# Performance work log

Hardware: AMD Instinct MI355X
Metric: run time of the kernel (lower is better)

## Reference

```python
import jax, jax.numpy as jnp
import numpy as np

HIDDEN = 128
IN_SIZE = 1
OUT_SIZE = 1
ENC_T = 8192
DEC_T = 4096


def _lstm_step(h, c, x, Wih, Whh, bih, bhh):
    # PyTorch LSTM gate order: i, f, g, o
    gates = Wih @ x + Whh @ h + bih + bhh  # [4H]
    i, f, g, o = jnp.split(gates, 4)
    c = jax.nn.sigmoid(f) * c + jax.nn.sigmoid(i) * jnp.tanh(g)
    h = jax.nn.sigmoid(o) * jnp.tanh(c)
    return h, c


def setup_inputs() -> dict:
    key = jax.random.key(0)
    ks = jax.random.split(key, 12)
    k = 1.0 / np.sqrt(HIDDEN)  # PyTorch default init bound
    u = lambda kk, shape: jax.random.uniform(kk, shape, jnp.float32, -k, k)
    return {
        "input_seq": jax.random.normal(ks[0], (ENC_T,), jnp.float32),
        "enc_Wih": u(ks[1], (4 * HIDDEN, IN_SIZE)),
        "enc_Whh": u(ks[2], (4 * HIDDEN, HIDDEN)),
        "enc_bih": u(ks[3], (4 * HIDDEN,)),
        "enc_bhh": u(ks[4], (4 * HIDDEN,)),
        "dec_Wih": u(ks[5], (4 * HIDDEN, OUT_SIZE)),
        "dec_Whh": u(ks[6], (4 * HIDDEN, HIDDEN)),
        "dec_bih": u(ks[7], (4 * HIDDEN,)),
        "dec_bhh": u(ks[8], (4 * HIDDEN,)),
        "fc_W": u(ks[9], (OUT_SIZE, HIDDEN)),
        "fc_b": u(ks[10], (OUT_SIZE,)),
        "target_seq_len": DEC_T,
    }


def reference(input_seq, enc_Wih, enc_Whh, enc_bih, enc_bhh,
              dec_Wih, dec_Whh, dec_bih, dec_bhh, fc_W, fc_b,
              target_seq_len):
    H = enc_Whh.shape[1]
    dt = input_seq.dtype

    def enc_step(carry, xt):
        h, c = carry
        h, c = _lstm_step(h, c, xt[None], enc_Wih, enc_Whh, enc_bih, enc_bhh)
        return (h, c), None

    (h, c), _ = jax.lax.scan(enc_step,
                             (jnp.zeros(H, dt), jnp.zeros(H, dt)),
                             input_seq)

    def dec_step(carry, _):
        h, c, y = carry  # y: previous prediction, shape [1]
        h, c = _lstm_step(h, c, y, dec_Wih, dec_Whh, dec_bih, dec_bhh)
        pred = fc_W @ h + fc_b  # [1]
        return (h, c, pred), pred

    _, preds = jax.lax.scan(dec_step, (h, c, jnp.zeros(1, dt)),
                            None, length=target_seq_len)
    # preds: [T_out, 1] -> torch.cat(outputs, dim=1) gives [1, T_out]
    return preds.T
```

## Files before the change

### kernel.cpp

```cpp
#include <hip/hip_runtime.h>


#define H      128
#define ENC_T  8192
#define DEC_T  4096
#define NT     512
#define NBLK   1
#define PSLICE 648

typedef float v2f __attribute__((ext_vector_type(2)));

__device__ __forceinline__ v2f pk_fma_s(v2f a, v2f b_sgpr, v2f c) {
    v2f d;
    asm("v_pk_fma_f32 %0, %1, %2, %3" : "=v"(d) : "v"(a), "s"(b_sgpr), "v"(c));
    return d;
}
__device__ __forceinline__ v2f pk_fma(v2f a, v2f b, v2f c) {
    v2f d;
    asm("v_pk_fma_f32 %0, %1, %2, %3" : "=v"(d) : "v"(a), "v"(b), "v"(c));
    return d;
}
__device__ __forceinline__ float sigm(float x) {
    return __builtin_amdgcn_rcpf(1.0f + __expf(-x));
}
__device__ __forceinline__ float tanhfast(float x) {
    return 1.0f - 2.0f * __builtin_amdgcn_rcpf(1.0f + __expf(2.0f * x));
}
__device__ __forceinline__ float rdlane(float v, int l) {
    return __int_as_float(__builtin_amdgcn_readlane(__float_as_int(v), l));
}
template <int CTRL>
__device__ __forceinline__ float qperm(float v) {
    return __int_as_float(
        __builtin_amdgcn_mov_dpp(__float_as_int(v), CTRL, 0xf, 0xf, true));
}

__global__ __launch_bounds__(NT, 2)
void seq2seq_lstm(const float* __restrict__ input_seq,
                  const float* __restrict__ enc_Wih,
                  const float* __restrict__ enc_Whh,
                  const float* __restrict__ enc_bih,
                  const float* __restrict__ enc_bhh,
                  const float* __restrict__ dec_Wih,
                  const float* __restrict__ dec_Whh,
                  const float* __restrict__ dec_bih,
                  const float* __restrict__ dec_bhh,
                  const float* __restrict__ fc_W,
                  const float* __restrict__ fc_b,
                  float* __restrict__ out,
                  unsigned* __restrict__ wsflag)
{
    (void)wsflag;
    __shared__ __align__(16) float xin[ENC_T];
    __shared__ __align__(16) float hbuf[2][H];
    __shared__ __align__(16) float part[2][8 * PSLICE];

    const int t    = threadIdx.x;
    const int lane = t & 63;
    const int wv   = t >> 6;
    const int jb   = 16 * wv;
    const int qq   = lane >> 2;
    const int g    = lane & 3;
    const int myu  = jb + qq;
    const int myrow = g * H + myu;
    const int prd  = 5 * myu + g;
    const int pwb  = wv * PSLICE + 5 * lane;

    {
        const float4* s = (const float4*)input_seq;
        float4* d = (float4*)xin;
        for (int i = t; i < ENC_T / 4; i += NT) d[i] = s[i];
    }

    v2f w2[8][8];
#pragma unroll
    for (int s = 0; s < 8; ++s) {
        const v2f* Wr = (const v2f*)(enc_Whh + (64 * s + lane) * H + jb);
#pragma unroll
        for (int jj = 0; jj < 8; ++jj) w2[s][jj] = Wr[jj];
    }
    float bias_r = enc_bih[myrow] + enc_bhh[myrow];
    float wih_r  = enc_Wih[myrow];

    float cst = 0.f;
    float hn  = 0.f;
    __syncthreads();

#define MATVEC(PB)                                                          \
    {                                                                       \
        v2f acc2[8];                                                        \
        _Pragma("unroll") for (int s = 0; s < 8; ++s)                       \
            acc2[s] = (v2f){0.f, 0.f};                                      \
        _Pragma("unroll") for (int jj = 0; jj < 8; ++jj) {                  \
            const float se = rdlane(hn, 8 * jj + 3);                        \
            const float so = rdlane(hn, 8 * jj + 7);                        \
            const v2f hp = {se, so};                                        \
            _Pragma("unroll") for (int s = 0; s < 8; ++s)                   \
                acc2[s] = pk_fma_s(w2[s][jj], hp, acc2[s]);                 \
        }                                                                   \
             \
        float* pb_ = &part[PB][pwb];                                        \
        pb_[0]   = acc2[0].x + acc2[0].y; pb_[320] = acc2[1].x + acc2[1].y; \
        pb_[1]   = acc2[2].x + acc2[2].y; pb_[321] = acc2[3].x + acc2[3].y; \
        pb_[2]   = acc2[4].x + acc2[4].y; pb_[322] = acc2[5].x + acc2[5].y; \
        pb_[3]   = acc2[6].x + acc2[6].y; pb_[323] = acc2[7].x + acc2[7].y; \
    }

#define REDUCE_UPDATE(PB, ABASE, STH)                                       \
    {                                                                       \
        const float p0 = part[PB][0 * PSLICE + prd];                        \
        const float p1 = part[PB][1 * PSLICE + prd];                        \
        const float p2 = part[PB][2 * PSLICE + prd];                        \
        const float p3 = part[PB][3 * PSLICE + prd];                        \
        const float p4 = part[PB][4 * PSLICE + prd];                        \
        const float p5 = part[PB][5 * PSLICE + prd];                        \
        const float p6 = part[PB][6 * PSLICE + prd];                        \
        const float p7 = part[PB][7 * PSLICE + prd];                        \
        const float a = (ABASE) + (((p0 + p1) + (p2 + p3)) +                \
                                   ((p4 + p5) + (p6 + p7)));                \
        const float v = (g == 2) ? tanhfast(a) : sigm(a);                   \
        const float vi = qperm<0x00>(v);                   \
        const float vf = qperm<0x55>(v);                   \
        const float vg = qperm<0xAA>(v);                   \
        const float vo = qperm<0xFF>(v);                   \
        cst = fmaf(vf, cst, vi * vg);                                       \
        hn  = vo * tanhfast(cst);                                           \
        if (STH && g == 3) hbuf[PB][myu] = hn;                              \
    }

    for (int st = 0; st < ENC_T; ++st) {
        const int pb = st & 1;
        MATVEC(pb);
        const float x = xin[st];
        __syncthreads();
        REDUCE_UPDATE(pb, fmaf(wih_r, x, bias_r), 0);
    }
    if (g == 3) hbuf[1][myu] = hn;

    const float fcb = fc_b[0];
    const float fwl = fc_W[lane];
    const float fwh = fc_W[64 + lane];
#pragma unroll
    for (int s = 0; s < 8; ++s) {
        const int r = 64 * s + lane;
        const float vi = dec_Wih[r];
        const v2f vip = {vi, vi};
        const v2f* Wr = (const v2f*)(dec_Whh + r * H + jb);
        const v2f* Fr = (const v2f*)(fc_W + jb);
#pragma unroll
        for (int jj = 0; jj < 8; ++jj)
            w2[s][jj] = pk_fma(vip, Fr[jj], Wr[jj]);
    }
    wih_r  = dec_Wih[myrow];
    bias_r = dec_bih[myrow] + dec_bhh[myrow] + wih_r * fcb;
    __syncthreads();
    float q0;
    {
        float p = fmaf(fwl, hbuf[1][lane], fwh * hbuf[1][64 + lane]);
        p += qperm<0xB1>(p);
        p += qperm<0x4E>(p);
#pragma unroll
        for (int m = 32; m >= 4; m >>= 1) p += __shfl_xor(p, m, 64);
        q0 = p + fcb;
    }
    float cb = bias_r - wih_r * q0;

    for (int st = 0; st < DEC_T; ++st) {
        const int pb = st & 1;
        MATVEC(pb);
        if (wv == 7 && st >= 2) {
            float p = fmaf(fwl, hbuf[pb][lane], fwh * hbuf[pb][64 + lane]);
            p += qperm<0xB1>(p);
            p += qperm<0x4E>(p);
#pragma unroll
            for (int m = 32; m >= 4; m >>= 1) p += __shfl_xor(p, m, 64);
            if (lane == 0) out[st - 2] = p + fcb;
        }
        __syncthreads();
        REDUCE_UPDATE(pb, cb, 1);
        cb = bias_r;
    }

    __syncthreads();
    if (wv == 7) {
        float p0 = fmaf(fwl, hbuf[0][lane], fwh * hbuf[0][64 + lane]);
        float p1 = fmaf(fwl, hbuf[1][lane], fwh * hbuf[1][64 + lane]);
#pragma unroll
        for (int m = 32; m >= 1; m >>= 1) {
            p0 += __shfl_xor(p0, m, 64);
            p1 += __shfl_xor(p1, m, 64);
        }
        if (lane == 0) {
            out[DEC_T - 2] = p0 + fcb;
            out[DEC_T - 1] = p1 + fcb;
        }
    }
}

extern "C" void kernel_launch(void* const* d_in, const int* in_sizes, int n_in,
                              void* d_out, int out_size, void* d_ws, size_t ws_size,
                              hipStream_t stream)
{
    (void)in_sizes; (void)n_in; (void)ws_size; (void)out_size;
    seq2seq_lstm<<<NBLK, NT, 0, stream>>>(
        (const float*)d_in[0],
        (const float*)d_in[1],
        (const float*)d_in[2],
        (const float*)d_in[3],
        (const float*)d_in[4],
        (const float*)d_in[5],
        (const float*)d_in[6],
        (const float*)d_in[7],
        (const float*)d_in[8],
        (const float*)d_in[9],
        (const float*)d_in[10],
        (float*)d_out,
        (unsigned*)d_ws);
}
```

Before: 8.680 ms.

## Interleave partial sums across warps so reduction uses two float4 LDS loads

Changes the shared-memory partial-sum layout so each output row's 8 per-warp partials are contiguous, with an XOR swizzle on the warp index to spread writes across banks. The reduce step then reads two float4 values instead of eight scalar loads. The step loops are unrolled by two with constant buffer indices, and the decoder's output projection is moved after the barrier so it reads the just-written hidden state, which shortens the output lag from two steps to one. This cuts LDS load instructions on the serial critical path, at the cost of more complex index math and possible write bank conflicts.

```diff
diff --git a/kernel.cpp b/kernel.cpp
--- a/kernel.cpp
+++ b/kernel.cpp
@@ -6,7 +6,7 @@
 #define DEC_T  4096
 #define NT     512
 #define NBLK   1
-#define PSLICE 648
+#define PBUF   5120
 
 typedef float v2f __attribute__((ext_vector_type(2)));
 
@@ -53,7 +53,7 @@
     (void)wsflag;
     __shared__ __align__(16) float xin[ENC_T];
     __shared__ __align__(16) float hbuf[2][H];
-    __shared__ __align__(16) float part[2][8 * PSLICE];
+    __shared__ __align__(16) float part[2][PBUF];
 
     const int t    = threadIdx.x;
     const int lane = t & 63;
@@ -63,8 +63,20 @@
     const int g    = lane & 3;
     const int myu  = jb + qq;
     const int myrow = g * H + myu;
-    const int prd  = 5 * myu + g;
-    const int pwb  = wv * PSLICE + 5 * lane;
+
+    const int prd = 5 * myu + g;
+    const int pA  = (prd >> 2) & 1;
+    const int rA  = 8 * prd + 4 * pA;
+    const int rB  = 8 * prd + 4 - 4 * pA;
+    int widx[8];
+    {
+        const int SOFF[8] = {0, 320, 1, 321, 2, 322, 3, 323};
+#pragma unroll
+        for (int s = 0; s < 8; ++s) {
+            const int pw = 5 * lane + SOFF[s];
+            widx[s] = 8 * pw + (wv ^ ((pw >> 2) & 7));
+        }
+    }
 
     {
         const float4* s = (const float4*)input_seq;
@@ -98,26 +110,20 @@
             _Pragma("unroll") for (int s = 0; s < 8; ++s)                   \
                 acc2[s] = pk_fma_s(w2[s][jj], hp, acc2[s]);                 \
         }                                                                   \
-             \
-        float* pb_ = &part[PB][pwb];                                        \
-        pb_[0]   = acc2[0].x + acc2[0].y; pb_[320] = acc2[1].x + acc2[1].y; \
-        pb_[1]   = acc2[2].x + acc2[2].y; pb_[321] = acc2[3].x + acc2[3].y; \
-        pb_[2]   = acc2[4].x + acc2[4].y; pb_[322] = acc2[5].x + acc2[5].y; \
-        pb_[3]   = acc2[6].x + acc2[6].y; pb_[323] = acc2[7].x + acc2[7].y; \
-    }
-
-#define REDUCE_UPDATE(PB, ABASE, STH)                                       \
+        float* pb_ = &part[PB][0];                                          \
+        _Pragma("unroll") for (int s = 0; s < 8; ++s)                       \
+            pb_[widx[s]] = acc2[s].x + acc2[s].y;                           \
+    }
+
+#define RED_LOAD(PB)                                                        \
+    const float4 a4_ = *(const float4*)&part[PB][rA];                       \
+    const float4 b4_ = *(const float4*)&part[PB][rB];
+
+#define RED_FIN(PB, ABASE, STH)                                             \
     {                                                                       \
-        const float p0 = part[PB][0 * PSLICE + prd];                        \
-        const float p1 = part[PB][1 * PSLICE + prd];                        \
-        const float p2 = part[PB][2 * PSLICE + prd];                        \
-        const float p3 = part[PB][3 * PSLICE + prd];                        \
-        const float p4 = part[PB][4 * PSLICE + prd];                        \
-        const float p5 = part[PB][5 * PSLICE + prd];                        \
-        const float p6 = part[PB][6 * PSLICE + prd];                        \
-        const float p7 = part[PB][7 * PSLICE + prd];                        \
-        const float a = (ABASE) + (((p0 + p1) + (p2 + p3)) +                \
-                                   ((p4 + p5) + (p6 + p7)));                \
+        const float a = (ABASE) +                                           \
+            (((a4_.x + a4_.y) + (a4_.z + a4_.w)) +                          \
+             ((b4_.x + b4_.y) + (b4_.z + b4_.w)));                          \
         const float v = (g == 2) ? tanhfast(a) : sigm(a);                   \
         const float vi = qperm<0x00>(v);                   \
         const float vf = qperm<0x55>(v);                   \
@@ -128,12 +134,31 @@
         if (STH && g == 3) hbuf[PB][myu] = hn;                              \
     }
 
-    for (int st = 0; st < ENC_T; ++st) {
-        const int pb = st & 1;
-        MATVEC(pb);
-        const float x = xin[st];
-        __syncthreads();
-        REDUCE_UPDATE(pb, fmaf(wih_r, x, bias_r), 0);
+#define OUTBLK(ST, HB)                                                      \
+    if (wv == 7 && (ST) >= 1) {                                             \
+        float p = fmaf(fwl, hbuf[HB][lane], fwh * hbuf[HB][64 + lane]);     \
+        p += qperm<0xB1>(p);                                     \
+        p += qperm<0x4E>(p);                                     \
+        _Pragma("unroll") for (int m = 32; m >= 4; m >>= 1)                 \
+            p += __shfl_xor(p, m, 64);                                      \
+        if (lane == 0) out[(ST) - 1] = p + fcb;                             \
+    }
+
+    for (int st = 0; st < ENC_T; st += 2) {
+        {
+            MATVEC(0);
+            const float x = xin[st];
+            __syncthreads();
+            RED_LOAD(0);
+            RED_FIN(0, fmaf(wih_r, x, bias_r), 0);
+        }
+        {
+            MATVEC(1);
+            const float x = xin[st + 1];
+            __syncthreads();
+            RED_LOAD(1);
+            RED_FIN(1, fmaf(wih_r, x, bias_r), 0);
+        }
     }
     if (g == 3) hbuf[1][myu] = hn;
 
@@ -165,35 +190,32 @@
     }
     float cb = bias_r - wih_r * q0;
 
-    for (int st = 0; st < DEC_T; ++st) {
-        const int pb = st & 1;
-        MATVEC(pb);
-        if (wv == 7 && st >= 2) {
-            float p = fmaf(fwl, hbuf[pb][lane], fwh * hbuf[pb][64 + lane]);
-            p += qperm<0xB1>(p);
-            p += qperm<0x4E>(p);
-#pragma unroll
-            for (int m = 32; m >= 4; m >>= 1) p += __shfl_xor(p, m, 64);
-            if (lane == 0) out[st - 2] = p + fcb;
-        }
-        __syncthreads();
-        REDUCE_UPDATE(pb, cb, 1);
-        cb = bias_r;
+    for (int st = 0; st < DEC_T; st += 2) {
+        {
+            MATVEC(0);
+            __syncthreads();
+            RED_LOAD(0);
+            OUTBLK(st, 1);
+            RED_FIN(0, cb, 1);
+            cb = bias_r;
+        }
+        {
+            MATVEC(1);
+            __syncthreads();
+            RED_LOAD(1);
+            OUTBLK(st + 1, 0);
+            RED_FIN(1, cb, 1);
+        }
     }
 
     __syncthreads();
     if (wv == 7) {
-        float p0 = fmaf(fwl, hbuf[0][lane], fwh * hbuf[0][64 + lane]);
-        float p1 = fmaf(fwl, hbuf[1][lane], fwh * hbuf[1][64 + lane]);
-#pragma unroll
-        for (int m = 32; m >= 1; m >>= 1) {
-            p0 += __shfl_xor(p0, m, 64);
-            p1 += __shfl_xor(p1, m, 64);
-        }
-        if (lane == 0) {
-            out[DEC_T - 2] = p0 + fcb;
-            out[DEC_T - 1] = p1 + fcb;
-        }
+        float p = fmaf(fwl, hbuf[1][lane], fwh * hbuf[1][64 + lane]);
+        p += qperm<0xB1>(p);
+        p += qperm<0x4E>(p);
+#pragma unroll
+        for (int m = 32; m >= 4; m >>= 1) p += __shfl_xor(p, m, 64);
+        if (lane == 0) out[DEC_T - 1] = p + fcb;
     }
 }
 
```

Result: faster. 8.124 ms (-6.4%).
